# Kernel tuning notes

Measured on AMD Instinct MI355X. Metric: run time of the kernel, lower is better.

## Reference

```python
import jax, jax.numpy as jnp
import numpy as np

P, L_T, B, N, D_S, D_T, H = 4, 12, 16, 197, 384, 768, 12
K = D_S // 4  # subspace_rank (calibration assumed done)
EPS_REG = 1e-4
CLAMP = 1.0 - 1e-7


def _orthogonal(key, rows, cols):
    # mimics nn.init.orthogonal_: QR of a gaussian, orthonormal rows (rows <= cols)
    a = jax.random.normal(key, (cols, rows), jnp.float32)
    q, r = jnp.linalg.qr(a)
    q = q * jnp.sign(jnp.diagonal(r))[None, :]
    return q.T  # [rows, cols], orthonormal rows


def _subspace(z, k):
    # z: [..., M, d] -> top-k eigenvectors of regularized covariance, [..., d, k]
    z = z - z.mean(axis=-2, keepdims=True)
    m = z.shape[-2]
    d = z.shape[-1]
    cov = jnp.einsum('...md,...me->...de', z, z) / m
    cov = cov + EPS_REG * jnp.eye(d, dtype=z.dtype)
    _, vecs = jnp.linalg.eigh(cov)  # ascending eigenvalues
    return vecs[..., -k:]


def setup_inputs() -> dict:
    key = jax.random.key(0)
    k0, k1, k2, k3, k4 = jax.random.split(key, 5)
    student_tokens = jax.random.normal(k0, (P, B, N, D_S), jnp.float32)
    teacher_tokens = jax.random.normal(k1, (L_T, B, N, D_T), jnp.float32)
    teacher_attns = jax.random.uniform(k2, (L_T, B, H, N, N), jnp.float32)
    proj_s = _orthogonal(k3, D_S, D_S)
    proj_t = _orthogonal(k4, D_S, D_T)
    log_temperatures = jnp.full((P,), float(np.log(np.e - 1.0)), jnp.float32)
    return {
        'student_tokens': student_tokens,
        'teacher_tokens': teacher_tokens,
        'teacher_attns': teacher_attns,
        'proj_s': proj_s,
        'proj_t': proj_t,
        'log_temperatures': log_temperatures,
    }


def reference(student_tokens, teacher_tokens, teacher_attns, proj_s, proj_t, log_temperatures):
    k = K
    lt = teacher_tokens.shape[0]
    p = student_tokens.shape[0]
    d_t = teacher_tokens.shape[-1]
    d_s = student_tokens.shape[-1]

    # teacher subspaces (torch.no_grad in original)
    z_t = teacher_tokens.reshape(lt, -1, d_t) @ proj_t.T          # [L, M, D_s]
    u_t = jax.lax.stop_gradient(_subspace(z_t, k))                 # [L, D_s, k]

    # student subspaces (differentiable)
    z_s = student_tokens.reshape(p, -1, d_s) @ proj_s.T            # [P, M, D_s]
    u_s = _subspace(z_s, k)                                        # [P, D_s, k]

    # principal angles between all (student layer, teacher layer) pairs
    m = jnp.einsum('pdi,ldj->plij', u_s, u_t)                      # [P, L, k, k]
    sigma = jnp.linalg.svd(m, compute_uv=False)                    # [P, L, k]
    theta = jnp.arccos(jnp.minimum(sigma, CLAMP))
    d_grass_sq = jnp.sum(theta * theta, axis=-1)                   # [P, L]

    tau = jax.nn.softplus(log_temperatures)                        # [P]
    weights = jax.nn.softmax(-d_grass_sq / (k * tau[:, None]), axis=1)  # [P, L]

    mixed = jnp.einsum('pl,lbnd->pbnd', weights, teacher_tokens)
    mixed_attn = jnp.einsum('pl,lbhnm->pbhnm', weights, teacher_attns)
    return mixed, mixed_attn
```

## Files before the change

### kernel.cpp

```cpp
#include <hip/hip_runtime.h>
#include <cstdint>
#include <cstddef>

#define PL 4
#define LL 12
#define NMAT 16
#define BB 16
#define SEQ 197
#define DS 384
#define DT 768
#define HEADS 12
#define MR 3152
#define KS 96
#define PD 144
#define EPSR 1e-4f
#define CLAMPF 0.99999988f

typedef long long i64;

__device__ __forceinline__ float hash01(uint32_t x){
  x ^= x >> 16; x *= 0x7feb352dU; x ^= x >> 15; x *= 0x846ca68bU; x ^= x >> 16;
  return (float)(x & 0xFFFFFFu) * (1.0f/8388608.0f) - 1.0f;
}
__device__ __forceinline__ float block_sum256(float v, float* red){
  for (int o = 32; o > 0; o >>= 1) v += __shfl_down(v, o);
  int t = threadIdx.x;
  if ((t & 63) == 0) red[t >> 6] = v;
  __syncthreads();
  float r = red[0] + red[1] + red[2] + red[3];
  __syncthreads();
  return r;
}
__device__ __forceinline__ float block_min256(float v, float* red){
  for (int o = 32; o > 0; o >>= 1) v = fminf(v, __shfl_down(v, o));
  int t = threadIdx.x;
  if ((t & 63) == 0) red[t >> 6] = v;
  __syncthreads();
  float r = fminf(fminf(red[0], red[1]), fminf(red[2], red[3]));
  __syncthreads();
  return r;
}
__device__ __forceinline__ float block_max256(float v, float* red){
  for (int o = 32; o > 0; o >>= 1) v = fmaxf(v, __shfl_down(v, o));
  int t = threadIdx.x;
  if ((t & 63) == 0) red[t >> 6] = v;
  __syncthreads();
  float r = fmaxf(fmaxf(red[0], red[1]), fmaxf(red[2], red[3]));
  __syncthreads();
  return r;
}
__device__ __forceinline__ int prow(int idx){
  int i = (int)((sqrtf(8.0f*(float)idx + 1.0f) - 1.0f)*0.5f);
  while ((i+1)*(i+2)/2 <= idx) i++;
  while (i*(i+1)/2 > idx) i--;
  return i;
}
__device__ __forceinline__ float gpiv(float q, float pm){
  return (fabsf(q) < pm) ? ((q < 0.f) ? -pm : pm) : q;
}
__device__ __forceinline__ float clampx(float x){
  return fminf(fmaxf(x, -1e15f), 1e15f);
}
__device__ __forceinline__ int sturm_count(const float* d, const float* e, int n, float x, float pm){
  float q = d[0] - x; int cnt = (q < 0.f) ? 1 : 0;
  for (int i = 1; i < n; i++){
    q = gpiv(q, pm);
    q = (d[i] - x) - e[i-1]*e[i-1]/q;
    cnt += (q < 0.f) ? 1 : 0;
  }
  return cnt;
}

__global__ __launch_bounds__(256) void k_zgemm(const float* __restrict__ A,
                                               const float* __restrict__ Pm,
                                               float* __restrict__ Z, int Kdim)
{
  __shared__ float As[16][68];
  __shared__ float Bs[16][132];
  const int t = threadIdx.x;
  const int bm = blockIdx.y * 64;
  const int bn = blockIdx.x * 128;
  const int tm = t >> 5;
  const int tn = t & 31;
  float acc[8][4];
#pragma unroll
  for (int i = 0; i < 8; i++)
#pragma unroll
    for (int j = 0; j < 4; j++) acc[i][j] = 0.f;

  for (int k0 = 0; k0 < Kdim; k0 += 16){
#pragma unroll
    for (int r = 0; r < 4; r++){
      int idx = t + r*256; int kk = idx & 15; int m = idx >> 4;
      As[kk][m] = A[(size_t)(bm+m)*Kdim + k0 + kk];
    }
#pragma unroll
    for (int r = 0; r < 8; r++){
      int idx = t + r*256; int kk = idx & 15; int n = idx >> 4;
      Bs[kk][n] = Pm[(size_t)(bn+n)*Kdim + k0 + kk];
    }
    __syncthreads();
#pragma unroll
    for (int kk = 0; kk < 16; kk++){
      float a[8], b[4];
#pragma unroll
      for (int i = 0; i < 8; i++) a[i] = As[kk][tm*8+i];
#pragma unroll
      for (int j = 0; j < 4; j++) b[j] = Bs[kk][tn*4+j];
#pragma unroll
      for (int i = 0; i < 8; i++)
#pragma unroll
        for (int j = 0; j < 4; j++) acc[i][j] += a[i]*b[j];
    }
    __syncthreads();
  }
#pragma unroll
  for (int i = 0; i < 8; i++){
    int row = bm + tm*8 + i;
#pragma unroll
    for (int j = 0; j < 4; j++)
      Z[(size_t)row*DS + bn + tn*4 + j] = acc[i][j];
  }
}

__global__ __launch_bounds__(256) void k_mu(const float* __restrict__ Z,
                                            float* __restrict__ mu, int mat0)
{
  int r0 = blockIdx.x * 16;
  int mat = mat0 + r0 / MR;
  int t = threadIdx.x;
  for (int c = t; c < DS; c += 256){
    float s = 0.f;
    for (int r = 0; r < 16; r++) s += Z[(size_t)(r0+r)*DS + c];
    unsafeAtomicAdd(&mu[mat*DS + c], s);
  }
}

__global__ __launch_bounds__(256) void k_cov(const float* __restrict__ Z,
                                             float* __restrict__ Gacc, int baseBatch)
{
  __shared__ float As[16][68];
  __shared__ float Bs[16][132];
  int bz = blockIdx.z; int b = bz >> 3; int ks = bz & 7;
  int k0s = ks * 394, k1 = k0s + 394;
  const float* Zb = Z + (size_t)b * MR * DS;
  int bi = blockIdx.y * 64, bj = blockIdx.x * 128;
  int t = threadIdx.x; int tm = t >> 5, tn = t & 31;
  float acc[8][4];
#pragma unroll
  for (int i = 0; i < 8; i++)
#pragma unroll
    for (int j = 0; j < 4; j++) acc[i][j] = 0.f;

  for (int k0 = k0s; k0 < k1; k0 += 16){
#pragma unroll
    for (int r = 0; r < 4; r++){
      int idx = t + r*256; int i = idx & 63; int kk = idx >> 6;
      int krow = k0 + kk;
      As[kk][i] = (krow < k1) ? Zb[(size_t)krow*DS + bi + i] : 0.f;
    }
#pragma unroll
    for (int r = 0; r < 8; r++){
      int idx = t + r*256; int j = idx & 127; int kk = idx >> 7;
      int krow = k0 + kk;
      Bs[kk][j] = (krow < k1) ? Zb[(size_t)krow*DS + bj + j] : 0.f;
    }
    __syncthreads();
#pragma unroll
    for (int kk = 0; kk < 16; kk++){
      float a[8], b[4];
#pragma unroll
      for (int i = 0; i < 8; i++) a[i] = As[kk][tm*8+i];
#pragma unroll
      for (int j = 0; j < 4; j++) b[j] = Bs[kk][tn*4+j];
#pragma unroll
      for (int i = 0; i < 8; i++)
#pragma unroll
        for (int j = 0; j < 4; j++) acc[i][j] += a[i]*b[j];
    }
    __syncthreads();
  }
  float* Gb = Gacc + (size_t)(baseBatch+b)*DS*DS;
#pragma unroll
  for (int i = 0; i < 8; i++){
    int row = bi + tm*8 + i;
#pragma unroll
    for (int j = 0; j < 4; j++)
      unsafeAtomicAdd(&Gb[(size_t)row*DS + bj + tn*4 + j], acc[i][j]);
  }
}

__global__ __launch_bounds__(256) void k_cov_epi(float* __restrict__ C, const float* __restrict__ mu)
{
  const float invM = 1.0f / (float)MR;
  size_t idx = (size_t)blockIdx.x * 256 + threadIdx.x;
  size_t total = (size_t)NMAT * DS * DS;
  if (idx >= total) return;
  int b = (int)(idx / (DS*DS));
  int rem = (int)(idx % (DS*DS));
  int r = rem / DS, c = rem % DS;
  float m1 = mu[b*DS + r] * invM;
  float m2 = mu[b*DS + c] * invM;
  float v = C[idx]*invM - m1*m2 + ((r == c) ? EPSR : 0.f);
  C[idx] = v;
}

__global__ __launch_bounds__(384) void k_lmax(const float* __restrict__ C, float* __restrict__ u_out)
{
  __shared__ float v[DS], w[DS], red[DS];
  int b = blockIdx.x, t = threadIdx.x;
  const float* Cb = C + (size_t)b*DS*DS;
  v[t] = hash01((uint32_t)(t*2654435761u + 12345u)) + 0.01f;
  __syncthreads();
  float lam = 1.0f;
  for (int it = 0; it < 16; it++){
    float s = 0.f;
    const float* row = Cb + (size_t)t*DS;
    for (int j = 0; j < DS; j++) s += row[j]*v[j];
    w[t] = s;
    __syncthreads();
    red[t] = s*s;
    __syncthreads();
    if (t < 128) red[t] += red[t+256];
    __syncthreads();
    for (int st = 128; st > 0; st >>= 1){
      if (t < st) red[t] += red[t+st];
      __syncthreads();
    }
    float nrm = sqrtf(fmaxf(red[0], 1e-30f));
    lam = nrm;
    v[t] = w[t] / nrm;
    __syncthreads();
  }
  if (t == 0) u_out[b] = 0.67f * lam;
}

__global__ __launch_bounds__(256) void k_omega(float* __restrict__ W)
{
  int idx = blockIdx.x*256 + threadIdx.x;
  W[idx] = hash01((uint32_t)idx * 2246822519u + 374761393u);
}

__global__ __launch_bounds__(256) void k_cheb(const float* __restrict__ A, int lda, i64 aBS,
                                              const float* __restrict__ Bm, int ldb, i64 bBS,
                                              float* __restrict__ out, i64 oBS,
                                              const float* __restrict__ tj,
                                              const float* __restrict__ prev,
                                              const float* __restrict__ u_arr,
                                              int Kdim, int Ncols, int mode)
{
  __shared__ float As[16][68];
  __shared__ float Bs[16][52];
  int b = blockIdx.z;
  const float* Ab = A + (size_t)b*aBS;
  const float* Bb = Bm + (size_t)b*bBS;
  int bm = blockIdx.y*64, bn = blockIdx.x*48;
  int t = threadIdx.x, tm = t >> 4, tn = t & 15;
  float acc[4][3];
#pragma unroll
  for (int i = 0; i < 4; i++)
#pragma unroll
    for (int j = 0; j < 3; j++) acc[i][j] = 0.f;

  for (int k0 = 0; k0 < Kdim; k0 += 16){
#pragma unroll
    for (int r = 0; r < 4; r++){
      int idx = t + r*256; int kk = idx & 15; int m = idx >> 4;
      As[kk][m] = Ab[(size_t)(bm+m)*lda + k0 + kk];
    }
#pragma unroll
    for (int r = 0; r < 3; r++){
      int idx = t + r*256; int n = idx % 48; int kk = idx / 48;
      Bs[kk][n] = Bb[(size_t)(k0+kk)*ldb + bn + n];
    }
    __syncthreads();
#pragma unroll
    for (int kk = 0; kk < 16; kk++){
      float a[4], bv[3];
#pragma unroll
      for (int i = 0; i < 4; i++) a[i] = As[kk][tm*4+i];
#pragma unroll
      for (int j = 0; j < 3; j++) bv[j] = Bs[kk][tn*3+j];
#pragma unroll
      for (int i = 0; i < 4; i++)
#pragma unroll
        for (int j = 0; j < 3; j++) acc[i][j] += a[i]*bv[j];
    }
    __syncthreads();
  }
  float uu = (mode == 0) ? 1.f : u_arr[b];
#pragma unroll
  for (int i = 0; i < 4; i++){
    int row = bm + tm*4 + i;
#pragma unroll
    for (int j = 0; j < 3; j++){
      int col = bn + tn*3 + j;
      size_t oidx = (size_t)b*oBS + (size_t)row*Ncols + col;
      float r;
      if (mode == 0)       r = acc[i][j];
      else if (mode == 1)  r = (2.f/uu)*acc[i][j] - prev[oidx];
      else                 r = (4.f/uu)*acc[i][j] - 2.f*tj[oidx] - prev[oidx];
      out[oidx] = r;
    }
  }
}

__global__ __launch_bounds__(256) void k_tn(const float* __restrict__ A, i64 aBS,
                                            const float* __restrict__ Bm, i64 bBS,
                                            float* __restrict__ out, i64 oBS,
                                            int Mdim, int Kdim, int pairMode)
{
  __shared__ float As[16][52], Bs[16][52];
  int b = blockIdx.z;
  const float *Ab, *Bb;
  if (pairMode){ int p = b/12, l = b%12; Ab = A + (size_t)(12+p)*aBS; Bb = Bm + (size_t)l*bBS; }
  else         { Ab = A + (size_t)b*aBS; Bb = Bm + (size_t)b*bBS; }
  int bi = blockIdx.y*48, bj = blockIdx.x*48;
  int t = threadIdx.x, tm = t >> 4, tn = t & 15;
  float acc[3][3];
#pragma unroll
  for (int i = 0; i < 3; i++)
#pragma unroll
    for (int j = 0; j < 3; j++) acc[i][j] = 0.f;

  for (int k0 = 0; k0 < Kdim; k0 += 16){
#pragma unroll
    for (int r = 0; r < 3; r++){
      int idx = t + r*256; int m = idx % 48; int kk = idx / 48;
      As[kk][m] = Ab[(size_t)(k0+kk)*Mdim + bi + m];
    }
#pragma unroll
    for (int r = 0; r < 3; r++){
      int idx = t + r*256; int n = idx % 48; int kk = idx / 48;
      Bs[kk][n] = Bb[(size_t)(k0+kk)*Mdim + bj + n];
    }
    __syncthreads();
#pragma unroll
    for (int kk = 0; kk < 16; kk++){
      float a[3], bv[3];
#pragma unroll
      for (int i = 0; i < 3; i++) a[i] = As[kk][tm*3+i];
#pragma unroll
      for (int j = 0; j < 3; j++) bv[j] = Bs[kk][tn*3+j];
#pragma unroll
      for (int i = 0; i < 3; i++)
#pragma unroll
        for (int j = 0; j < 3; j++) acc[i][j] += a[i]*bv[j];
    }
    __syncthreads();
  }
#pragma unroll
  for (int i = 0; i < 3; i++)
#pragma unroll
    for (int j = 0; j < 3; j++)
      out[(size_t)b*oBS + (size_t)(bi+tm*3+i)*Mdim + bj + tn*3 + j] = acc[i][j];
}

__global__ __launch_bounds__(256) void k_chol(const float* __restrict__ G, i64 gBS,
                                              float* __restrict__ Rout, i64 rBS,
                                              int n, float ridge)
{
  __shared__ float Cp[PD*(PD+1)/2];
  __shared__ float dinv[PD];
  int b = blockIdx.x, t = threadIdx.x;
  const float* Gb = G + (size_t)b*gBS;
  int pcount = n*(n+1)/2;
  for (int j = t; j < n; j += 256) dinv[j] = rsqrtf(fmaxf(Gb[(size_t)j*n+j], 1e-30f));
  __syncthreads();
  for (int idx = t; idx < pcount; idx += 256){
    int i = prow(idx); int j = idx - i*(i+1)/2;
    float g = Gb[(size_t)i*n+j]*dinv[i]*dinv[j];
    if (i == j) g += ridge;
    Cp[idx] = g;
  }
  __syncthreads();
  for (int j = 0; j < n; j++){
    int dj = j*(j+1)/2 + j;
    if (t == 0){
      float s = Cp[dj];
      Cp[dj] = (s > 1e-9f) ? sqrtf(s) : 1e12f;
    }
    __syncthreads();
    float Ljj = Cp[dj];
    for (int i = j+1+t; i < n; i += 256) Cp[i*(i+1)/2+j] /= Ljj;
    __syncthreads();
    for (int i = j+1+t; i < n; i += 256){
      int bi2 = i*(i+1)/2;
      float Lij = Cp[bi2+j];
      for (int c = j+1; c <= i; c++) Cp[bi2+c] -= Lij * Cp[c*(c+1)/2+j];
    }
    __syncthreads();
  }
  float* Rb = Rout + (size_t)b*rBS;
  for (int idx = t; idx < pcount; idx += 256) Rb[idx] = Cp[idx];
  for (int j = t; j < n; j += 256) Rb[pcount+j] = dinv[j];
}

__global__ __launch_bounds__(64) void k_trisolve(float* __restrict__ W, i64 wBS, int rowsPerBatch,
                                                 const float* __restrict__ Rp, i64 rBS, int n)
{
  __shared__ float rowb[64][145];
  int t = threadIdx.x;
  int grow = blockIdx.x*64 + t;
  int b = grow / rowsPerBatch, r = grow % rowsPerBatch;
  const float* Lb = Rp + (size_t)b*rBS;
  const float* dinv = Lb + n*(n+1)/2;
  float* Wrow = W + (size_t)b*wBS + (size_t)r*n;
  for (int j = 0; j < n; j++) rowb[t][j] = Wrow[j]*dinv[j];
  for (int j = 0; j < n; j++){
    int base = j*(j+1)/2;
    float s = rowb[t][j];
    for (int i = 0; i < j; i++) s -= Lb[base+i]*rowb[t][i];
    rowb[t][j] = s / Lb[base+j];
  }
  for (int j = 0; j < n; j++) Wrow[j] = rowb[t][j];
}

__device__ void tridiag_packed(float* Ap, int n, float* d, float* e, float* bet,
                               float* v1, float* w1, float* red)
{
  int t = threadIdx.x;
  for (int k = 0; k < n-2; k++){
    int base_k1 = (k+1)*(k+2)/2;
    float p = 0.f;
    for (int i = k+2+t; i < n; i += 256){ float x = Ap[i*(i+1)/2+k]; p += x*x; }
    float sigma = block_sum256(p, red);
    float alpha = Ap[base_k1 + k];
    float ek, beta, vfirst;
    if (sigma < 1e-28f){ ek = alpha; beta = 0.f; vfirst = 0.f; }
    else {
      float nu = sqrtf(alpha*alpha + sigma);
      ek = (alpha >= 0.f) ? -nu : nu;
      vfirst = alpha - ek;
      beta = 1.f/(nu*(nu + fabsf(alpha)));
    }
    if (t == 0){ d[k] = Ap[k*(k+1)/2+k]; e[k] = ek; bet[k] = beta; Ap[base_k1+k] = vfirst; }
    for (int i = k+1+t; i < n; i += 256) v1[i] = (i == k+1) ? vfirst : Ap[i*(i+1)/2+k];
    __syncthreads();
    if (beta != 0.f){
      for (int i = k+1+t; i < n; i += 256){
        int bi2 = i*(i+1)/2;
        float s = 0.f;
        for (int j = k+1; j <= i; j++) s += Ap[bi2+j]*v1[j];
        for (int j = i+1; j < n; j++)  s += Ap[j*(j+1)/2+i]*v1[j];
        w1[i] = beta*s;
      }
      __syncthreads();
      p = 0.f;
      for (int i = k+1+t; i < n; i += 256) p += w1[i]*v1[i];
      float wv = block_sum256(p, red);
      float Kw = 0.5f*beta*wv;
      for (int i = k+1+t; i < n; i += 256) w1[i] -= Kw*v1[i];
      __syncthreads();
      for (int i = k+1+t; i < n; i += 256){
        int bi2 = i*(i+1)/2;
        float vi = v1[i], wi = w1[i];
        for (int j = k+1; j <= i; j++) Ap[bi2+j] -= vi*w1[j] + wi*v1[j];
      }
      __syncthreads();
    }
  }
  if (t == 0){
    int n2 = n-2, n1 = n-1;
    d[n2] = Ap[n2*(n2+1)/2+n2];
    e[n2] = Ap[n1*(n1+1)/2+n2];
    d[n1] = Ap[n1*(n1+1)/2+n1];
    bet[n2] = 0.f; bet[n1] = 0.f; e[n1] = 0.f;
  }
  __syncthreads();
}

__global__ __launch_bounds__(256) void k_tridiagB(const float* __restrict__ Bg,
                                                  float* __restrict__ Bh,
                                                  float* __restrict__ betg,
                                                  float* __restrict__ deg)
{
  __shared__ float Ap[PD*(PD+1)/2];
  __shared__ float d[PD], e[PD], bet[PD], v1[PD], w1[PD], red[8];
  int b = blockIdx.x, t = threadIdx.x;
  const float* Bb = Bg + (size_t)b*PD*PD;
  const int pc = PD*(PD+1)/2;
  for (int idx = t; idx < pc; idx += 256){
    int i = prow(idx); int j = idx - i*(i+1)/2;
    Ap[idx] = 0.5f*(Bb[i*PD+j] + Bb[j*PD+i]);
  }
  __syncthreads();
  tridiag_packed(Ap, PD, d, e, bet, v1, w1, red);
  for (int idx = t; idx < pc; idx += 256) Bh[(size_t)b*pc + idx] = Ap[idx];
  for (int i = t; i < PD; i += 256){
    betg[b*PD + i] = bet[i];
    deg[b*2*PD + i] = d[i];
    deg[b*2*PD + PD + i] = e[i];
  }
}

__global__ __launch_bounds__(256) void k_invit(const float* __restrict__ deg, float* __restrict__ Yg)
{
  __shared__ float d[PD], e[PD], lam[KS], red[8];
  __shared__ float bounds[2];
  __shared__ float tw[2][48][PD+1];
  int b = blockIdx.x, t = threadIdx.x;
  for (int i = t; i < PD; i += 256){ d[i] = deg[b*2*PD + i]; e[i] = deg[b*2*PD + PD + i]; }
  __syncthreads();
  float lo = 1e30f, hi = -1e30f;
  for (int i = t; i < PD; i += 256){
    float ea = (i > 0) ? fabsf(e[i-1]) : 0.f;
    float eb = (i < PD-1) ? fabsf(e[i]) : 0.f;
    lo = fminf(lo, d[i]-ea-eb); hi = fmaxf(hi, d[i]+ea+eb);
  }
  lo = block_min256(lo, red);
  hi = block_max256(hi, red);
  if (t == 0){ bounds[0] = lo - 1e-5f; bounds[1] = hi + 1e-5f; }
  __syncthreads();
  const float pm = 1e-12f;
  if (t < KS){
    int target = (PD - KS) + t;
    float a = bounds[0], bb2 = bounds[1];
    for (int it = 0; it < 34; it++){
      float mid = 0.5f*(a+bb2);
      int cnt = sturm_count(d, e, PD, mid, pm);
      if (cnt > target) bb2 = mid; else a = mid;
    }
    lam[t] = 0.5f*(a+bb2);
  }
  __syncthreads();
  if (t == 0){
    float scale = fmaxf(fabsf(lam[0]), fabsf(lam[KS-1])) + 1e-20f;
    int pos = 0;
    for (int v = 1; v < KS; v++){
      if (lam[v] - lam[v-1] < 2e-5f*scale){ pos++; lam[v] += (float)pos*4e-6f*scale; }
      else pos = 0;
    }
  }
  __syncthreads();
  float* Yb = Yg + (size_t)b*PD*KS;
  for (int batch = 0; batch < 2; batch++){
    if (t < 48){
      int v = batch*48 + t;
      float L = lam[v];
      float* pF = tw[0][t];
      float* sb = tw[1][t];
      pF[0] = gpiv(d[0]-L, pm);
      for (int i = 1; i < PD; i++) pF[i] = gpiv((d[i]-L) - e[i-1]*e[i-1]/pF[i-1], pm);
      sb[PD-1] = gpiv(d[PD-1]-L, pm);
      for (int i = PD-2; i >= 0; i--) sb[i] = gpiv((d[i]-L) - e[i]*e[i]/sb[i+1], pm);
      int r = 0; float best = 1e30f;
      for (int i = 0; i < PD; i++){
        float g = fabsf(pF[i] + sb[i] - (d[i]-L));
        if (g < best){ best = g; r = i; }
      }
      pF[r] = 1.f;
      for (int i = r-1; i >= 0; i--){
        float xi = -e[i]*pF[i+1]/pF[i];
        pF[i] = clampx(xi);
      }
      for (int i = r+1; i < PD; i++){
        float xm1 = (i-1 == r) ? 1.f : sb[i-1];
        float xi = -e[i-1]*xm1/sb[i];
        sb[i] = clampx(xi);
      }
      float nn = 0.f;
      for (int i = 0; i <= r; i++) nn += pF[i]*pF[i];
      for (int i = r+1; i < PD; i++) nn += sb[i]*sb[i];
      float inv = rsqrtf(fmaxf(nn, 1e-30f));
      for (int i = 0; i <= r; i++) Yb[(size_t)i*KS + v] = pF[i]*inv;
      for (int i = r+1; i < PD; i++) Yb[(size_t)i*KS + v] = sb[i]*inv;
    }
    __syncthreads();
  }
}

__global__ __launch_bounds__(256) void k_backxf(const float* __restrict__ Bh,
                                                const float* __restrict__ betg,
                                                float* __restrict__ Yg)
{
  __shared__ float sY[PD][KS+1];
  __shared__ float v1[PD], tf[KS], part[2][KS];
  int b = blockIdx.x, t = threadIdx.x;
  float* Yb = Yg + (size_t)b*PD*KS;
  const float* Bhb = Bh + (size_t)b*(PD*(PD+1)/2);
  const float* betb = betg + b*PD;
  for (int idx = t; idx < PD*KS; idx += 256){ sY[idx/KS][idx%KS] = Yb[idx]; }
  __syncthreads();
  for (int k = PD-3; k >= 0; k--){
    float beta = betb[k];
    if (beta == 0.f) continue;
    for (int i = k+1+t; i < PD; i += 256) v1[i] = Bhb[i*(i+1)/2+k];
    __syncthreads();
    int mlen = PD-1-k;
    if (t < 2*KS){
      int c = t % KS, h = t / KS;
      int half = (mlen+1)/2;
      int i0 = k+1 + h*half;
      int i1 = (h == 0) ? (k+1+half) : PD;
      float s = 0.f;
      for (int i = i0; i < i1; i++) s += v1[i]*sY[i][c];
      part[h][c] = s;
    }
    __syncthreads();
    if (t < KS) tf[t] = beta*(part[0][t] + part[1][t]);
    __syncthreads();
    for (int idx = t; idx < mlen*KS; idx += 256){
      int i = k+1 + idx/KS, c = idx % KS;
      sY[i][c] -= v1[i]*tf[c];
    }
    __syncthreads();
  }
  for (int idx = t; idx < PD*KS; idx += 256) Yb[idx] = sY[idx/KS][idx%KS];
}

__global__ __launch_bounds__(256) void k_sigma(const float* __restrict__ Mg, float* __restrict__ d2g)
{
  __shared__ float sM[KS][KS+1];
  __shared__ float Gp[KS*(KS+1)/2];
  __shared__ float d[KS], e[KS], bet[KS], v1[KS], w1[KS], red[8];
  __shared__ float bounds[2];
  int b = blockIdx.x, t = threadIdx.x;
  const float* Mb = Mg + (size_t)b*KS*KS;
  for (int idx = t; idx < KS*KS; idx += 256) sM[idx/KS][idx%KS] = Mb[idx];
  __syncthreads();
  const int pc = KS*(KS+1)/2;
  for (int idx = t; idx < pc; idx += 256){
    int a = prow(idx); int c = idx - a*(a+1)/2;
    float s = 0.f;
    for (int i = 0; i < KS; i++) s += sM[i][a]*sM[i][c];
    Gp[idx] = s;
  }
  __syncthreads();
  tridiag_packed(Gp, KS, d, e, bet, v1, w1, red);
  float lo = 1e30f, hi = -1e30f;
  for (int i = t; i < KS; i += 256){
    float ea = (i > 0) ? fabsf(e[i-1]) : 0.f;
    float eb = (i < KS-1) ? fabsf(e[i]) : 0.f;
    lo = fminf(lo, d[i]-ea-eb); hi = fmaxf(hi, d[i]+ea+eb);
  }
  lo = block_min256(lo, red);
  hi = block_max256(hi, red);
  if (t == 0){ bounds[0] = lo - 1e-6f; bounds[1] = hi + 1e-6f; }
  __syncthreads();
  const float pm = 1e-12f;
  float th2 = 0.f;
  if (t < KS){
    float a = bounds[0], bb2 = bounds[1];
    for (int it = 0; it < 34; it++){
      float mid = 0.5f*(a+bb2);
      int cnt = sturm_count(d, e, KS, mid, pm);
      if (cnt > t) bb2 = mid; else a = mid;
    }
    float L = 0.5f*(a+bb2);
    float sig = sqrtf(fmaxf(L, 0.f));
    sig = fminf(sig, CLAMPF);
    float th = acosf(sig);
    th2 = th*th;
  }
  float total = block_sum256(th2, red);
  if (t == 0) d2g[b] = total;
}

__global__ void k_weights(const float* __restrict__ d2, const float* __restrict__ lt,
                          float* __restrict__ w)
{
  int t = threadIdx.x;
  if (t < PL){
    float tau = log1pf(expf(lt[t]));
    float denom = (float)KS * tau;
    float lg[LL]; float mx = -1e30f;
    for (int l = 0; l < LL; l++){ lg[l] = -d2[t*LL+l]/denom; mx = fmaxf(mx, lg[l]); }
    float s = 0.f;
    for (int l = 0; l < LL; l++){ lg[l] = expf(lg[l]-mx); s += lg[l]; }
    for (int l = 0; l < LL; l++) w[t*LL+l] = lg[l]/s;
  }
}

__global__ __launch_bounds__(256) void k_mix_tok(const float* __restrict__ tt,
                                                 const float* __restrict__ w,
                                                 float* __restrict__ out)
{
  __shared__ float sw[PL*LL];
  if (threadIdx.x < PL*LL) sw[threadIdx.x] = w[threadIdx.x];
  __syncthreads();
  const size_t N4 = (size_t)BB*SEQ*DT/4;
  const float4* t4 = (const float4*)tt;
  float4* o4 = (float4*)out;
  for (size_t i = (size_t)blockIdx.x*256 + threadIdx.x; i < N4; i += (size_t)gridDim.x*256){
    float4 a[PL];
#pragma unroll
    for (int p = 0; p < PL; p++){ a[p].x = 0; a[p].y = 0; a[p].z = 0; a[p].w = 0; }
    for (int l = 0; l < LL; l++){
      float4 v = t4[(size_t)l*N4 + i];
#pragma unroll
      for (int p = 0; p < PL; p++){
        float ww = sw[p*LL+l];
        a[p].x += ww*v.x; a[p].y += ww*v.y; a[p].z += ww*v.z; a[p].w += ww*v.w;
      }
    }
#pragma unroll
    for (int p = 0; p < PL; p++) o4[(size_t)p*N4 + i] = a[p];
  }
}

__global__ __launch_bounds__(256) void k_mix_attn(const float* __restrict__ at,
                                                  const float* __restrict__ w,
                                                  float* __restrict__ out)
{
  __shared__ float sw[PL*LL];
  if (threadIdx.x < PL*LL) sw[threadIdx.x] = w[threadIdx.x];
  __syncthreads();
  const size_t N4 = (size_t)BB*HEADS*SEQ*SEQ/4;
  const float4* t4 = (const float4*)at;
  float4* o4 = (float4*)out;
  for (size_t i = (size_t)blockIdx.x*256 + threadIdx.x; i < N4; i += (size_t)gridDim.x*256){
    float4 a[PL];
#pragma unroll
    for (int p = 0; p < PL; p++){ a[p].x = 0; a[p].y = 0; a[p].z = 0; a[p].w = 0; }
    for (int l = 0; l < LL; l++){
      float4 v = t4[(size_t)l*N4 + i];
#pragma unroll
      for (int p = 0; p < PL; p++){
        float ww = sw[p*LL+l];
        a[p].x += ww*v.x; a[p].y += ww*v.y; a[p].z += ww*v.z; a[p].w += ww*v.w;
      }
    }
#pragma unroll
    for (int p = 0; p < PL; p++) o4[(size_t)p*N4 + i] = a[p];
  }
}

extern "C" void kernel_launch(void* const* d_in, const int* in_sizes, int n_in,
                              void* d_out, int out_size, void* d_ws, size_t ws_size,
                              hipStream_t stream)
{
  const float* student = (const float*)d_in[0];
  const float* teacher = (const float*)d_in[1];
  const float* attns   = (const float*)d_in[2];
  const float* proj_s  = (const float*)d_in[3];
  const float* proj_t  = (const float*)d_in[4];
  const float* logtemp = (const float*)d_in[5];
  float* out = (float*)d_out;

  const size_t o_Z   = 0;
  const size_t o_C   = o_Z   + (size_t)4*MR*DS;
  const size_t o_Wa  = o_C   + (size_t)NMAT*DS*DS;
  const size_t o_Wb  = o_Wa  + (size_t)NMAT*DS*PD;
  const size_t o_G   = o_Wb  + (size_t)NMAT*DS*PD;
  const size_t o_R   = o_G   + (size_t)NMAT*PD*PD;
  const size_t o_B   = o_R   + (size_t)NMAT*(PD*(PD+1)/2 + PD);
  const size_t o_Bh  = o_B   + (size_t)NMAT*PD*PD;
  const size_t o_bet = o_Bh  + (size_t)NMAT*(PD*(PD+1)/2);
  const size_t o_de  = o_bet + (size_t)NMAT*PD;
  const size_t o_Y   = o_de  + (size_t)NMAT*2*PD;
  const size_t o_U   = o_Y   + (size_t)NMAT*PD*KS;
  const size_t o_M   = o_U   + (size_t)NMAT*DS*KS;
  const size_t o_mu  = o_M   + (size_t)48*KS*KS;
  const size_t o_u   = o_mu  + (size_t)NMAT*DS;
  const size_t o_sm  = o_u   + 16;
  const size_t TOTAL = o_sm + 96;
  const size_t NEED_BYTES = TOTAL*sizeof(float);

  bool ws_ok = (ws_size >= NEED_BYTES);
  float* base = ws_ok ? (float*)d_ws : (float*)d_out;
  float* Zb  = base + o_Z;
  float* Cp  = base + o_C;
  float* Wa  = base + o_Wa;
  float* Wb  = base + o_Wb;
  float* Gp_ = base + o_G;
  float* Rp_ = base + o_R;
  float* Bp_ = base + o_B;
  float* Bh_ = base + o_Bh;
  float* bet_= base + o_bet;
  float* de_ = base + o_de;
  float* Y_  = base + o_Y;
  float* U_  = base + o_U;
  float* Mp_ = base + o_M;
  float* mu_ = base + o_mu;
  float* up_ = base + o_u;
  float* d2_ = ws_ok ? (base + o_sm) : (float*)d_ws;
  float* w_  = d2_ + 48;

  hipMemsetAsync(mu_, 0, (size_t)NMAT*DS*sizeof(float), stream);
  hipMemsetAsync(Cp, 0, (size_t)NMAT*DS*DS*sizeof(float), stream);

  for (int ch = 0; ch < 4; ch++){
    const float* src; const float* proj; int Kdim; int mat0;
    if (ch < 3){ src = teacher + (size_t)ch*4*MR*DT; proj = proj_t; Kdim = DT; mat0 = ch*4; }
    else       { src = student;                      proj = proj_s; Kdim = DS; mat0 = 12; }
    k_zgemm<<<dim3(3,197), 256, 0, stream>>>(src, proj, Zb, Kdim);
    k_mu<<<788, 256, 0, stream>>>(Zb, mu_, mat0);
    k_cov<<<dim3(3,6,32), 256, 0, stream>>>(Zb, Cp, mat0);
  }
  k_cov_epi<<<9216, 256, 0, stream>>>(Cp, mu_);
  k_lmax<<<NMAT, 384, 0, stream>>>(Cp, up_);

  k_omega<<<(NMAT*DS*PD)/256, 256, 0, stream>>>(Wa);
  const dim3 gch(3, 6, NMAT);
  const i64 wS = (i64)DS*PD, cS = (i64)DS*DS;

  k_cheb<<<gch,256,0,stream>>>(Cp, DS, cS, Wa, PD, wS, Wb, wS, nullptr, Wa, up_, DS, PD, 1);
  {
    float* Tprev = Wa; float* Tcur = Wb;
    for (int j = 2; j <= 7; j++){
      k_cheb<<<gch,256,0,stream>>>(Cp, DS, cS, Tcur, PD, wS, Tprev, wS, Tcur, Tprev, up_, DS, PD, 2);
      float* tmp = Tprev; Tprev = Tcur; Tcur = tmp;
    }
  }
  const i64 rS = (i64)(PD*(PD+1)/2 + PD);
  auto cholqr = [&](float* W, float ridge){
    k_tn<<<dim3(3,3,NMAT),256,0,stream>>>(W, wS, W, wS, Gp_, (i64)PD*PD, PD, DS, 0);
    k_chol<<<NMAT,256,0,stream>>>(Gp_, (i64)PD*PD, Rp_, rS, PD, ridge);
    k_trisolve<<<(NMAT*DS)/64,64,0,stream>>>(W, wS, DS, Rp_, rS, PD);
  };
  cholqr(Wb, 3e-6f);

  k_cheb<<<gch,256,0,stream>>>(Cp, DS, cS, Wb, PD, wS, Wa, wS, nullptr, Wb, up_, DS, PD, 1);
  {
    float* Tprev = Wb; float* Tcur = Wa;
    for (int j = 2; j <= 7; j++){
      k_cheb<<<gch,256,0,stream>>>(Cp, DS, cS, Tcur, PD, wS, Tprev, wS, Tcur, Tprev, up_, DS, PD, 2);
      float* tmp = Tprev; Tprev = Tcur; Tcur = tmp;
    }
  }
  cholqr(Wa, 3e-6f);
  cholqr(Wa, 1e-7f);

  k_cheb<<<gch,256,0,stream>>>(Cp, DS, cS, Wa, PD, wS, Wb, wS, nullptr, nullptr, up_, DS, PD, 0);
  k_tn<<<dim3(3,3,NMAT),256,0,stream>>>(Wa, wS, Wb, wS, Bp_, (i64)PD*PD, PD, DS, 0);

  k_tridiagB<<<NMAT,256,0,stream>>>(Bp_, Bh_, bet_, de_);
  k_invit<<<NMAT,256,0,stream>>>(de_, Y_);
  k_backxf<<<NMAT,256,0,stream>>>(Bh_, bet_, Y_);

  const i64 r96S = (i64)(KS*(KS+1)/2 + KS);
  k_tn<<<dim3(2,2,NMAT),256,0,stream>>>(Y_, (i64)PD*KS, Y_, (i64)PD*KS, Gp_, (i64)KS*KS, KS, PD, 0);
  k_chol<<<NMAT,256,0,stream>>>(Gp_, (i64)KS*KS, Rp_, r96S, KS, 1e-6f);
  k_trisolve<<<(NMAT*PD)/64,64,0,stream>>>(Y_, (i64)PD*KS, PD, Rp_, r96S, KS);

  k_cheb<<<dim3(2,6,NMAT),256,0,stream>>>(Wa, PD, wS, Y_, KS, (i64)PD*KS, U_, (i64)DS*KS,
                                          nullptr, nullptr, up_, PD, KS, 0);
  k_tn<<<dim3(2,2,48),256,0,stream>>>(U_, (i64)DS*KS, U_, (i64)DS*KS, Mp_, (i64)KS*KS, KS, DS, 1);
  k_sigma<<<48,256,0,stream>>>(Mp_, d2_);
  k_weights<<<1,64,0,stream>>>(d2_, logtemp, w_);

  k_mix_tok<<<2364,256,0,stream>>>(teacher, w_, out);
  k_mix_attn<<<4096,256,0,stream>>>(attns, w_, out + (size_t)PL*BB*SEQ*DT);
}
```

Baseline: 9.233 ms.

## Store tridiagonalization matrices in full padded LDS layout with float4 updates

Householder tridiagonalization now works on a full row-major matrix with padded stride in shared memory instead of packed lower-triangular storage. This lets the matrix-vector product and the rank-2 update use contiguous float4 loads. The packed form needed index arithmetic and strided, uncoalesced column access. The Gram matrix M^T M in k_sigma is moved out of the serial per-block loop into a separate batched k_tn launch, and the stored Householder vectors are now full rows, so backxf indexing and the workspace layout change to match. The cost is more LDS (about 85KB for the 144 case), which may limit occupancy, plus redundant work on the full symmetric matrix.

```diff
diff --git a/kernel.cpp b/kernel.cpp
--- a/kernel.cpp
+++ b/kernel.cpp
@@ -16,6 +16,9 @@
 #define EPSR 1e-4f
 #define CLAMPF 0.99999988f
 
+#define TLDA 148
+#define SLDA 100
+
 typedef long long i64;
 
 __device__ __forceinline__ float hash01(uint32_t x){
@@ -416,16 +419,17 @@
   for (int j = 0; j < n; j++) Wrow[j] = rowb[t][j];
 }
 
-__device__ void tridiag_packed(float* Ap, int n, float* d, float* e, float* bet,
-                               float* v1, float* w1, float* red)
-{
-  int t = threadIdx.x;
+__device__ void tridiag_full(float* A, int n, int lda,
+                             float* d, float* e, float* bet,
+                             float* w1, float* red)
+{
+  const int t = threadIdx.x;
   for (int k = 0; k < n-2; k++){
-    int base_k1 = (k+1)*(k+2)/2;
+    float* rowk = A + (size_t)k*lda;
+    float alpha = rowk[k+1];
     float p = 0.f;
-    for (int i = k+2+t; i < n; i += 256){ float x = Ap[i*(i+1)/2+k]; p += x*x; }
+    for (int i = k+2+t; i < n; i += 256){ float x = rowk[i]; p += x*x; }
     float sigma = block_sum256(p, red);
-    float alpha = Ap[base_k1 + k];
     float ek, beta, vfirst;
     if (sigma < 1e-28f){ ek = alpha; beta = 0.f; vfirst = 0.f; }
     else {
@@ -434,37 +438,54 @@
       vfirst = alpha - ek;
       beta = 1.f/(nu*(nu + fabsf(alpha)));
     }
-    if (t == 0){ d[k] = Ap[k*(k+1)/2+k]; e[k] = ek; bet[k] = beta; Ap[base_k1+k] = vfirst; }
-    for (int i = k+1+t; i < n; i += 256) v1[i] = (i == k+1) ? vfirst : Ap[i*(i+1)/2+k];
+    if (t == 0){ d[k] = rowk[k]; e[k] = ek; bet[k] = beta; rowk[k+1] = vfirst; }
     __syncthreads();
     if (beta != 0.f){
       for (int i = k+1+t; i < n; i += 256){
-        int bi2 = i*(i+1)/2;
+        const float* rowi = A + (size_t)i*lda;
         float s = 0.f;
-        for (int j = k+1; j <= i; j++) s += Ap[bi2+j]*v1[j];
-        for (int j = i+1; j < n; j++)  s += Ap[j*(j+1)/2+i]*v1[j];
+        int j = k+1;
+        int j1 = (k+4) & ~3; if (j1 > n) j1 = n;
+        for (; j < j1; j++) s += rowi[j]*rowk[j];
+#pragma unroll 4
+        for (; j < n; j += 4){
+          float4 a4 = *(const float4*)(rowi + j);
+          float4 v4 = *(const float4*)(rowk + j);
+          s += a4.x*v4.x + a4.y*v4.y + a4.z*v4.z + a4.w*v4.w;
+        }
         w1[i] = beta*s;
       }
       __syncthreads();
-      p = 0.f;
-      for (int i = k+1+t; i < n; i += 256) p += w1[i]*v1[i];
-      float wv = block_sum256(p, red);
+      float pp = 0.f;
+      for (int i = k+1+t; i < n; i += 256) pp += w1[i]*rowk[i];
+      float wv = block_sum256(pp, red);
       float Kw = 0.5f*beta*wv;
-      for (int i = k+1+t; i < n; i += 256) w1[i] -= Kw*v1[i];
+      for (int i = k+1+t; i < n; i += 256) w1[i] -= Kw*rowk[i];
       __syncthreads();
+      int j0 = (k+1) & ~3;
       for (int i = k+1+t; i < n; i += 256){
-        int bi2 = i*(i+1)/2;
-        float vi = v1[i], wi = w1[i];
-        for (int j = k+1; j <= i; j++) Ap[bi2+j] -= vi*w1[j] + wi*v1[j];
+        float* rowi = A + (size_t)i*lda;
+        float vi = rowk[i], wi = w1[i];
+#pragma unroll 4
+        for (int j = j0; j < n; j += 4){
+          float4 a4 = *(float4*)(rowi + j);
+          float4 w4 = *(const float4*)(w1 + j);
+          float4 v4 = *(const float4*)(rowk + j);
+          a4.x -= vi*w4.x + wi*v4.x;
+          a4.y -= vi*w4.y + wi*v4.y;
+          a4.z -= vi*w4.z + wi*v4.z;
+          a4.w -= vi*w4.w + wi*v4.w;
+          *(float4*)(rowi + j) = a4;
+        }
       }
       __syncthreads();
     }
   }
   if (t == 0){
     int n2 = n-2, n1 = n-1;
-    d[n2] = Ap[n2*(n2+1)/2+n2];
-    e[n2] = Ap[n1*(n1+1)/2+n2];
-    d[n1] = Ap[n1*(n1+1)/2+n1];
+    d[n2] = A[(size_t)n2*lda+n2];
+    e[n2] = A[(size_t)n1*lda+n2];
+    d[n1] = A[(size_t)n1*lda+n1];
     bet[n2] = 0.f; bet[n1] = 0.f; e[n1] = 0.f;
   }
   __syncthreads();
@@ -475,18 +496,26 @@
                                                   float* __restrict__ betg,
                                                   float* __restrict__ deg)
 {
-  __shared__ float Ap[PD*(PD+1)/2];
-  __shared__ float d[PD], e[PD], bet[PD], v1[PD], w1[PD], red[8];
+  extern __shared__ float smem[];
+  float* A   = smem;
+  float* d   = A   + PD*TLDA;
+  float* e   = d   + PD;
+  float* bet = e   + PD;
+  float* w1  = bet + PD;
+  float* red = w1  + PD;
   int b = blockIdx.x, t = threadIdx.x;
   const float* Bb = Bg + (size_t)b*PD*PD;
-  const int pc = PD*(PD+1)/2;
-  for (int idx = t; idx < pc; idx += 256){
-    int i = prow(idx); int j = idx - i*(i+1)/2;
-    Ap[idx] = 0.5f*(Bb[i*PD+j] + Bb[j*PD+i]);
-  }
-  __syncthreads();
-  tridiag_packed(Ap, PD, d, e, bet, v1, w1, red);
-  for (int idx = t; idx < pc; idx += 256) Bh[(size_t)b*pc + idx] = Ap[idx];
+  for (int idx = t; idx < PD*PD; idx += 256){
+    int i = idx / PD, j = idx - i*PD;
+    A[i*TLDA + j] = 0.5f*(Bb[idx] + Bb[j*PD + i]);
+  }
+  __syncthreads();
+  tridiag_full(A, PD, TLDA, d, e, bet, w1, red);
+  float* Bhb = Bh + (size_t)b*PD*PD;
+  for (int idx = t; idx < PD*PD; idx += 256){
+    int i = idx / PD, j = idx - i*PD;
+    Bhb[idx] = A[i*TLDA + j];
+  }
   for (int i = t; i < PD; i += 256){
     betg[b*PD + i] = bet[i];
     deg[b*2*PD + i] = d[i];
@@ -578,14 +607,14 @@
   __shared__ float v1[PD], tf[KS], part[2][KS];
   int b = blockIdx.x, t = threadIdx.x;
   float* Yb = Yg + (size_t)b*PD*KS;
-  const float* Bhb = Bh + (size_t)b*(PD*(PD+1)/2);
+  const float* Bhb = Bh + (size_t)b*PD*PD;
   const float* betb = betg + b*PD;
   for (int idx = t; idx < PD*KS; idx += 256){ sY[idx/KS][idx%KS] = Yb[idx]; }
   __syncthreads();
   for (int k = PD-3; k >= 0; k--){
     float beta = betb[k];
     if (beta == 0.f) continue;
-    for (int i = k+1+t; i < PD; i += 256) v1[i] = Bhb[i*(i+1)/2+k];
+    for (int i = k+1+t; i < PD; i += 256) v1[i] = Bhb[(size_t)k*PD + i];
     __syncthreads();
     int mlen = PD-1-k;
     if (t < 2*KS){
@@ -609,25 +638,19 @@
   for (int idx = t; idx < PD*KS; idx += 256) Yb[idx] = sY[idx/KS][idx%KS];
 }
 
-__global__ __launch_bounds__(256) void k_sigma(const float* __restrict__ Mg, float* __restrict__ d2g)
-{
-  __shared__ float sM[KS][KS+1];
-  __shared__ float Gp[KS*(KS+1)/2];
-  __shared__ float d[KS], e[KS], bet[KS], v1[KS], w1[KS], red[8];
+__global__ __launch_bounds__(256) void k_sigma(const float* __restrict__ Gg, float* __restrict__ d2g)
+{
+  __shared__ __align__(16) float A[KS*SLDA];
+  __shared__ float d[KS], e[KS], bet[KS], w1[KS], red[8];
   __shared__ float bounds[2];
   int b = blockIdx.x, t = threadIdx.x;
-  const float* Mb = Mg + (size_t)b*KS*KS;
-  for (int idx = t; idx < KS*KS; idx += 256) sM[idx/KS][idx%KS] = Mb[idx];
-  __syncthreads();
-  const int pc = KS*(KS+1)/2;
-  for (int idx = t; idx < pc; idx += 256){
-    int a = prow(idx); int c = idx - a*(a+1)/2;
-    float s = 0.f;
-    for (int i = 0; i < KS; i++) s += sM[i][a]*sM[i][c];
-    Gp[idx] = s;
-  }
-  __syncthreads();
-  tridiag_packed(Gp, KS, d, e, bet, v1, w1, red);
+  const float* Gb = Gg + (size_t)b*KS*KS;
+  for (int idx = t; idx < KS*KS; idx += 256){
+    int i = idx / KS, j = idx - i*KS;
+    A[i*SLDA + j] = 0.5f*(Gb[idx] + Gb[(size_t)j*KS + i]);
+  }
+  __syncthreads();
+  tridiag_full(A, KS, SLDA, d, e, bet, w1, red);
   float lo = 1e30f, hi = -1e30f;
   for (int i = t; i < KS; i += 256){
     float ea = (i > 0) ? fabsf(e[i-1]) : 0.f;
@@ -746,7 +769,7 @@
   const size_t o_R   = o_G   + (size_t)NMAT*PD*PD;
   const size_t o_B   = o_R   + (size_t)NMAT*(PD*(PD+1)/2 + PD);
   const size_t o_Bh  = o_B   + (size_t)NMAT*PD*PD;
-  const size_t o_bet = o_Bh  + (size_t)NMAT*(PD*(PD+1)/2);
+  const size_t o_bet = o_Bh  + (size_t)NMAT*PD*PD;
   const size_t o_de  = o_bet + (size_t)NMAT*PD;
   const size_t o_Y   = o_de  + (size_t)NMAT*2*PD;
   const size_t o_U   = o_Y   + (size_t)NMAT*PD*KS;
@@ -825,7 +848,10 @@
   k_cheb<<<gch,256,0,stream>>>(Cp, DS, cS, Wa, PD, wS, Wb, wS, nullptr, nullptr, up_, DS, PD, 0);
   k_tn<<<dim3(3,3,NMAT),256,0,stream>>>(Wa, wS, Wb, wS, Bp_, (i64)PD*PD, PD, DS, 0);
 
-  k_tridiagB<<<NMAT,256,0,stream>>>(Bp_, Bh_, bet_, de_);
+  {
+    const size_t tridiag_lds = (size_t)(PD*TLDA + 4*PD + 8) * sizeof(float);
+    k_tridiagB<<<NMAT,256,tridiag_lds,stream>>>(Bp_, Bh_, bet_, de_);
+  }
   k_invit<<<NMAT,256,0,stream>>>(de_, Y_);
   k_backxf<<<NMAT,256,0,stream>>>(Bh_, bet_, Y_);
 
@@ -837,7 +863,8 @@
   k_cheb<<<dim3(2,6,NMAT),256,0,stream>>>(Wa, PD, wS, Y_, KS, (i64)PD*KS, U_, (i64)DS*KS,
                                           nullptr, nullptr, up_, PD, KS, 0);
   k_tn<<<dim3(2,2,48),256,0,stream>>>(U_, (i64)DS*KS, U_, (i64)DS*KS, Mp_, (i64)KS*KS, KS, DS, 1);
-  k_sigma<<<48,256,0,stream>>>(Mp_, d2_);
+  k_tn<<<dim3(2,2,48),256,0,stream>>>(Mp_, (i64)KS*KS, Mp_, (i64)KS*KS, Wa, (i64)KS*KS, KS, KS, 0);
+  k_sigma<<<48,256,0,stream>>>(Wa, d2_);
   k_weights<<<1,64,0,stream>>>(d2_, logtemp, w_);
 
   k_mix_tok<<<2364,256,0,stream>>>(teacher, w_, out);
```

After: 8.302 ms. 10.1% less time.
